# Kernel optimization log

Hardware: AMD Instinct MI355X
Metric: run time of the kernel (lower is better)

## Reference

```python
import jax, jax.numpy as jnp
import numpy as np

B, T, D = 64, 512, 512
K_CODES = 256
K_FUTURE = 2


def _gru(x, w_ih, w_hh, b_ih, b_hh):
    # x: [B,T,D]; PyTorch GRU gate order: r, z, n; weights [3D, D]
    xg = jnp.einsum('btd,gd->btg', x, w_ih) + b_ih  # [B,T,3D] precomputed input gates

    def step(h, xg_t):
        hg = h @ w_hh.T + b_hh                      # [B,3D]
        xr, xz, xn = jnp.split(xg_t, 3, axis=-1)
        hr, hz, hn = jnp.split(hg, 3, axis=-1)
        r = jax.nn.sigmoid(xr + hr)
        z = jax.nn.sigmoid(xz + hz)
        n = jnp.tanh(xn + r * hn)
        h_new = (1.0 - z) * n + z * h
        return h_new, h_new

    h0 = jnp.zeros((x.shape[0], w_hh.shape[1]), x.dtype)
    _, hs = jax.lax.scan(step, h0, jnp.swapaxes(xg, 0, 1))
    return jnp.swapaxes(hs, 0, 1)  # [B,T,D]


def setup_inputs() -> dict:
    key = jax.random.key(0)
    ks = jax.random.split(key, 8)
    return {
        'features': jax.random.normal(ks[0], (B, T, D), jnp.float32),
        'codebook': jax.random.uniform(ks[1], (K_CODES, D), jnp.float32, -0.1, 0.1),
        'w_ih': jax.random.normal(ks[2], (3 * D, D), jnp.float32) * 0.02,
        'w_hh': jax.random.normal(ks[3], (3 * D, D), jnp.float32) * 0.02,
        'b_ih': jax.random.normal(ks[4], (3 * D,), jnp.float32) * 0.02,
        'b_hh': jax.random.normal(ks[5], (3 * D,), jnp.float32) * 0.02,
        'proj_w': jax.random.normal(ks[6], (D, D), jnp.float32) * 0.02,
        'proj_b': jax.random.normal(ks[7], (D,), jnp.float32) * 0.02,
    }


def reference(features, codebook, w_ih, w_hh, b_ih, b_hh, proj_w, proj_b):
    b, t, d = features.shape
    # --- quantize: cdist + argmin + gather (squared dists give same argmin) ---
    flat = features.reshape(-1, d)                              # [B*T, D]
    d2 = (jnp.sum(flat * flat, axis=1, keepdims=True)
          - 2.0 * flat @ codebook.T
          + jnp.sum(codebook * codebook, axis=1))               # [B*T, K]
    indices = jnp.argmin(d2, axis=1)                            # [B*T]
    quantized = codebook[indices].reshape(b, t, d)              # gather
    indices = indices.reshape(b, t)

    # --- context prediction loss ---
    hidden = _gru(quantized, w_ih, w_hh, b_ih, b_hh)            # [B,T,D]
    context_proj = hidden @ proj_w.T + proj_b                   # [B,T,D]
    k_max = min(K_FUTURE, t - 1)
    cp_loss = jnp.float32(0.0)
    for k in range(1, k_max + 1):
        cp_loss = cp_loss + jnp.mean((context_proj[:, :-k] - features[:, k:]) ** 2)
    cp_loss = cp_loss / k_max

    # --- VQ loss (stop_gradient mirrors torch .detach()) ---
    commitment_loss = jnp.mean((jax.lax.stop_gradient(features) - quantized) ** 2)
    codebook_loss = jnp.mean((features - jax.lax.stop_gradient(quantized)) ** 2)
    vq_loss = commitment_loss + 0.25 * codebook_loss

    total_loss = cp_loss + vq_loss
    return quantized, indices, total_loss, cp_loss, vq_loss
```

## Files before the change

kernel.cpp:

```cpp
#include <hip/hip_runtime.h>
#include <hip/hip_bf16.h>

#define B_ 64
#define T_ 512
#define D_ 512
#define K_ 256
#define G3 1536

typedef __attribute__((ext_vector_type(8))) short sh8;
typedef __attribute__((ext_vector_type(4))) short sh4;
typedef __attribute__((ext_vector_type(4))) float fx4;
typedef __attribute__((ext_vector_type(4))) int   ix4;

__device__ __forceinline__ short f2bf(float x) {
  __hip_bfloat16 h = __float2bfloat16(x);
  union { __hip_bfloat16 h; short s; } u; u.h = h; return u.s;
}
__device__ __forceinline__ float sigm(float x) { return 1.f / (1.f + __expf(-x)); }
__device__ __forceinline__ float tanh_fast(float x) {
  float e2 = __expf(-2.f * x);
  return (1.f - e2) / (1.f + e2);
}

__global__ void k_cnorm(const float* __restrict__ cb, double* __restrict__ cn) {
  int c = threadIdx.x;
  if (c < K_) {
    double s = 0.0;
    for (int k = 0; k < D_; ++k) { double v = cb[c * D_ + k]; s += v * v; }
    cn[c] = s;
  }
}

__global__ __launch_bounds__(256) void k_cg(const float* __restrict__ cb,
                                            const float* __restrict__ wih,
                                            const float* __restrict__ bih,
                                            const float* __restrict__ bhh,
                                            float* __restrict__ cg) {
  __shared__ float wl[16][512];
  int j0 = blockIdx.x * 16, c0 = blockIdx.y * 64;
  for (int v = threadIdx.x; v < 16 * 128; v += 256) {
    int r = v >> 7, q = v & 127;
    *(fx4*)&wl[r][q * 4] = *(const fx4*)&wih[(j0 + r) * D_ + q * 4];
  }
  __syncthreads();
  for (int p = threadIdx.x; p < 1024; p += 256) {
    int j = p >> 6, c = c0 + (p & 63);
    fx4 a = {0.f, 0.f, 0.f, 0.f};
    const float* cbr = &cb[c * D_];
    for (int q = 0; q < 128; ++q) {
      fx4 w4 = *(fx4*)&wl[j][q * 4];
      fx4 c4 = *(const fx4*)&cbr[q * 4];
      a += w4 * c4;
    }
    int jg = j0 + j;
    float bias = bih[jg] + (jg < 1024 ? bhh[jg] : 0.f);
    cg[c * G3 + jg] = ((a.x + a.y) + (a.z + a.w)) + bias;
  }
}

__global__ void k_cvt(const float* __restrict__ src, __hip_bfloat16* __restrict__ dst, int n4) {
  int i = blockIdx.x * blockDim.x + threadIdx.x;
  if (i < n4) {
    fx4 v = *(const fx4*)&src[i * 4];
    sh4 o; o[0] = f2bf(v.x); o[1] = f2bf(v.y); o[2] = f2bf(v.z); o[3] = f2bf(v.w);
    *(sh4*)&dst[i * 4] = o;
  }
}

__global__ __launch_bounds__(256) void k_quant(const float* __restrict__ feat,
                                               const float* __restrict__ cb,
                                               const double* __restrict__ cn,
                                               int* __restrict__ idxw,
                                               float* __restrict__ outq,
                                               float* __restrict__ outi,
                                               double* __restrict__ lacc) {
  __shared__ float fl[16][516];
  __shared__ double ss1[16][16], ss2[16][16];
  __shared__ int ii1[16][16], ii2[16][16];
  __shared__ int idxl[16];
  __shared__ float rsv[4];
  int row0 = blockIdx.x * 16;
  int tid = threadIdx.x;
  for (int v = tid; v < 16 * 128; v += 256) {
    int r = v >> 7, q = v & 127;
    *(fx4*)&fl[r][q * 4] = *(const fx4*)&feat[(row0 + r) * D_ + q * 4];
  }
  __syncthreads();
  int r = tid & 15, g = tid >> 4;
  fx4 acc[16];
#pragma unroll
  for (int c = 0; c < 16; ++c) acc[c] = (fx4){0.f, 0.f, 0.f, 0.f};
  for (int ch = 0; ch < 8; ++ch) {
    fx4 fc[16];
#pragma unroll
    for (int q = 0; q < 16; ++q) fc[q] = *(fx4*)&fl[r][ch * 64 + q * 4];
#pragma unroll
    for (int c = 0; c < 16; ++c) {
      const float* cbp = &cb[(g * 16 + c) * D_ + ch * 64];
#pragma unroll
      for (int q = 0; q < 16; ++q) {
        fx4 c4 = *(const fx4*)&cbp[q * 4];
        acc[c] += fc[q] * c4;
      }
    }
  }
  double b1 = 1e300, b2 = 1e300; int i1 = 0, i2 = 0;
#pragma unroll
  for (int c = 0; c < 16; ++c) {
    int ci = g * 16 + c;
    double dot = (double)acc[c].x + acc[c].y + acc[c].z + acc[c].w;
    double s = cn[ci] - 2.0 * dot;
    if (s < b1) { b2 = b1; i2 = i1; b1 = s; i1 = ci; }
    else if (s < b2) { b2 = s; i2 = ci; }
  }
  ss1[r][g] = b1; ss2[r][g] = b2; ii1[r][g] = i1; ii2[r][g] = i2;
  __syncthreads();
  if (tid < 16) {
    int rr = tid;
    double c1 = 1e300, c2 = 1e300; int j1 = 0, j2 = 0;
    for (int g2 = 0; g2 < 16; ++g2) {
      double s = ss1[rr][g2]; int ix = ii1[rr][g2];
      if (s < c1 || (s == c1 && ix < j1)) { c2 = c1; j2 = j1; c1 = s; j1 = ix; }
      else if (s < c2 || (s == c2 && ix < j2)) { c2 = s; j2 = ix; }
      s = ss2[rr][g2]; ix = ii2[rr][g2];
      if (s < c1 || (s == c1 && ix < j1)) { c2 = c1; j2 = j1; c1 = s; j1 = ix; }
      else if (s < c2 || (s == c2 && ix < j2)) { c2 = s; j2 = ix; }
    }
    int pick = j1;
    if (c2 - c1 < 1e-4) {
      double d1 = 0.0, d2 = 0.0;
      for (int k = 0; k < D_; ++k) {
        double fv = fl[rr][k];
        d1 += fv * (double)cb[j1 * D_ + k];
        d2 += fv * (double)cb[j2 * D_ + k];
      }
      double e1 = cn[j1] - 2.0 * d1, e2 = cn[j2] - 2.0 * d2;
      if (e2 < e1 || (e2 == e1 && j2 < j1)) pick = j2;
    }
    idxl[rr] = pick;
    idxw[row0 + rr] = pick;
    outi[row0 + rr] = (float)pick;
  }
  __syncthreads();
  float vs = 0.f;
  for (int v = tid; v < 16 * 128; v += 256) {
    int rr = v >> 7, q = v & 127;
    fx4 c4 = *(const fx4*)&cb[idxl[rr] * D_ + q * 4];
    *(fx4*)&outq[(row0 + rr) * D_ + q * 4] = c4;
    fx4 f4 = *(fx4*)&fl[rr][q * 4];
    fx4 d = f4 - c4;
    vs += d.x * d.x + d.y * d.y + d.z * d.z + d.w * d.w;
  }
#pragma unroll
  for (int off = 32; off > 0; off >>= 1) vs += __shfl_down(vs, off);
  if ((tid & 63) == 0) rsv[tid >> 6] = vs;
  __syncthreads();
  if (tid == 0) atomicAdd(&lacc[2], (double)(rsv[0] + rsv[1] + rsv[2] + rsv[3]));
}

__global__ __launch_bounds__(256, 1) void k_gru(const float* __restrict__ whh,
                                                const float* __restrict__ bhh,
                                                const float* __restrict__ cg,
                                                const int* __restrict__ idx,
                                                __hip_bfloat16* __restrict__ hid,
                                                unsigned int* __restrict__ flag,
                                                int* __restrict__ xcca,
                                                unsigned int* __restrict__ bar0) {
  int bid = blockIdx.x;
  int g = bid & 7, s = bid >> 3;
  int tid = threadIdx.x;
  int w = tid >> 6, lane = tid & 63, l15 = lane & 15, l4 = lane >> 4;

  sh8 A0[16], A1[16], A2[16];
#pragma unroll
  for (int kt = 0; kt < 16; ++kt) {
#pragma unroll
    for (int t3 = 0; t3 < 3; ++t3) {
      const float* wr = &whh[((t3 * 512) + s * 64 + w * 16 + l15) * D_];
      int k0 = kt * 32 + l4 * 8;
      fx4 x = *(const fx4*)&wr[k0];
      fx4 y = *(const fx4*)&wr[k0 + 4];
      sh8 tt;
      tt[0] = f2bf(x.x); tt[1] = f2bf(x.y); tt[2] = f2bf(x.z); tt[3] = f2bf(x.w);
      tt[4] = f2bf(y.x); tt[5] = f2bf(y.y); tt[6] = f2bf(y.z); tt[7] = f2bf(y.w);
      if (t3 == 0) A0[kt] = tt; else if (t3 == 1) A1[kt] = tt; else A2[kt] = tt;
    }
  }

  const bool act = (l15 < 8);
  const int b = l15;
  const int dg0 = s * 64 + w * 16 + l4 * 4;

  fx4 bn = *(const fx4*)&bhh[1024 + dg0];
  fx4 hp = {0.f, 0.f, 0.f, 0.f};

  __shared__ int sh_fast;
  if (tid == 0) {
    int xcc = 0;
    asm volatile("s_getreg_b32 %0, hwreg(HW_REG_XCC_ID)" : "=s"(xcc));
    __hip_atomic_store(&xcca[bid], xcc, __ATOMIC_RELEASE, __HIP_MEMORY_SCOPE_AGENT);
    __hip_atomic_fetch_add(bar0, 1u, __ATOMIC_ACQ_REL, __HIP_MEMORY_SCOPE_AGENT);
    while (__hip_atomic_load(bar0, __ATOMIC_ACQUIRE, __HIP_MEMORY_SCOPE_AGENT) < 64u)
      __builtin_amdgcn_s_sleep(2);
    int x0 = __hip_atomic_load(&xcca[g], __ATOMIC_RELAXED, __HIP_MEMORY_SCOPE_AGENT);
    int f = 1;
    for (int m = 1; m < 8; ++m)
      if (__hip_atomic_load(&xcca[g + 8 * m], __ATOMIC_RELAXED, __HIP_MEMORY_SCOPE_AGENT) != x0)
        f = 0;
    sh_fast = f;
    __threadfence();
  }
  __syncthreads();
  const bool fast = (sh_fast != 0);

  for (int t = 0; t < T_; ++t) {
    fx4 cr = {0, 0, 0, 0}, cz = {0, 0, 0, 0}, cnn = {0, 0, 0, 0};
    if (act) {
      int ci = idx[(g * 8 + b) * T_ + t];
      const float* cgr = &cg[(size_t)ci * G3 + dg0];
      cr  = *(const fx4*)cgr;
      cz  = *(const fx4*)(cgr + 512);
      cnn = *(const fx4*)(cgr + 1024);
    }

    fx4 a0 = {0, 0, 0, 0}, a1 = {0, 0, 0, 0}, a2 = {0, 0, 0, 0};
    if (t > 0) {
      if (tid < 8) {
        const unsigned* fp = &flag[(tid * 8 + g) * 32];
        while (__hip_atomic_load(fp, __ATOMIC_RELAXED, __HIP_MEMORY_SCOPE_AGENT)
               < (unsigned)t) {}
      }
      if (!fast && tid == 0) __threadfence();
      __syncthreads();

      const __hip_bfloat16* hrow =
          &hid[((size_t)(g * 8 + (l15 & 7)) * T_ + (t - 1)) * D_];
#pragma unroll
      for (int kt = 0; kt < 16; ++kt) {
        sh8 bfr = {0, 0, 0, 0, 0, 0, 0, 0};
        if (act) bfr = *(const sh8*)&hrow[kt * 32 + l4 * 8];
        a0 = __builtin_amdgcn_mfma_f32_16x16x32_bf16(A0[kt], bfr, a0, 0, 0, 0);
        a1 = __builtin_amdgcn_mfma_f32_16x16x32_bf16(A1[kt], bfr, a1, 0, 0, 0);
        a2 = __builtin_amdgcn_mfma_f32_16x16x32_bf16(A2[kt], bfr, a2, 0, 0, 0);
      }
    }

    if (act) {
      sh4 hb4;
#pragma unroll
      for (int rg = 0; rg < 4; ++rg) {
        float rr = sigm(cr[rg] + a0[rg]);
        float zz = sigm(cz[rg] + a1[rg]);
        float nn = tanh_fast(cnn[rg] + rr * (a2[rg] + bn[rg]));
        float hv = (1.f - zz) * nn + zz * hp[rg];
        hp[rg] = hv;
        hb4[rg] = f2bf(hv);
      }
      *(sh4*)&hid[((size_t)(g * 8 + b) * T_ + t) * D_ + dg0] = hb4;
    }
    __syncthreads();
    if (tid == 0) {
      if (!fast) __threadfence();
      __hip_atomic_store(&flag[bid * 32], (unsigned)(t + 1), __ATOMIC_RELAXED,
                         __HIP_MEMORY_SCOPE_AGENT);
    }
  }
}

__global__ __launch_bounds__(256) void k_proj(const __hip_bfloat16* __restrict__ hid,
                                              const __hip_bfloat16* __restrict__ pwb,
                                              const float* __restrict__ pb,
                                              const float* __restrict__ feat,
                                              double* __restrict__ lacc) {
  __shared__ char Bl[512 * 64];
  __shared__ char Al[32 * 64];
  __shared__ float rs1[4], rs2[4];
  int Mb = blockIdx.x * 32;
  int tid = threadIdx.x;
  int w = tid >> 6, lane = tid & 63, l15 = lane & 15, l4 = lane >> 4;
  fx4 acc[2][8];
#pragma unroll
  for (int a = 0; a < 2; ++a)
#pragma unroll
    for (int b = 0; b < 8; ++b) acc[a][b] = (fx4){0, 0, 0, 0};

  for (int kc = 0; kc < 16; ++kc) {
    for (int v = tid; v < 2048; v += 256) {
      int rw = v >> 2, sg = v & 3;
      ix4 d = *(const ix4*)&pwb[rw * D_ + kc * 32 + sg * 8];
      *(ix4*)(Bl + rw * 64 + ((sg * 16) ^ ((rw & 7) << 4))) = d;
    }
    if (tid < 128) {
      int rw = tid >> 2, sg = tid & 3;
      ix4 d = *(const ix4*)&hid[(size_t)(Mb + rw) * D_ + kc * 32 + sg * 8];
      *(ix4*)(Al + rw * 64 + ((sg * 16) ^ ((rw & 7) << 4))) = d;
    }
    __syncthreads();
    sh8 af0, af1;
    {
      int m = l15;
      af0 = *(const sh8*)(Al + m * 64 + ((l4 * 16) ^ ((m & 7) << 4)));
      m = 16 + l15;
      af1 = *(const sh8*)(Al + m * 64 + ((l4 * 16) ^ ((m & 7) << 4)));
    }
#pragma unroll
    for (int nt = 0; nt < 8; ++nt) {
      int n = (w * 8 + nt) * 16 + l15;
      sh8 bf = *(const sh8*)(Bl + n * 64 + ((l4 * 16) ^ ((n & 7) << 4)));
      acc[0][nt] = __builtin_amdgcn_mfma_f32_16x16x32_bf16(af0, bf, acc[0][nt], 0, 0, 0);
      acc[1][nt] = __builtin_amdgcn_mfma_f32_16x16x32_bf16(af1, bf, acc[1][nt], 0, 0, 0);
    }
    __syncthreads();
  }

  float s1 = 0.f, s2 = 0.f;
#pragma unroll
  for (int mt = 0; mt < 2; ++mt) {
#pragma unroll
    for (int nt = 0; nt < 8; ++nt) {
      int n = (w * 8 + nt) * 16 + l15;
      float bias = pb[n];
#pragma unroll
      for (int rg = 0; rg < 4; ++rg) {
        int m = Mb + mt * 16 + l4 * 4 + rg;
        float val = acc[mt][nt][rg] + bias;
        int t = m & (T_ - 1);
        if (t < T_ - 1) { float d = val - feat[(size_t)(m + 1) * D_ + n]; s1 += d * d; }
        if (t < T_ - 2) { float d = val - feat[(size_t)(m + 2) * D_ + n]; s2 += d * d; }
      }
    }
  }
#pragma unroll
  for (int off = 32; off > 0; off >>= 1) {
    s1 += __shfl_down(s1, off);
    s2 += __shfl_down(s2, off);
  }
  if (lane == 0) { rs1[w] = s1; rs2[w] = s2; }
  __syncthreads();
  if (tid == 0) {
    atomicAdd(&lacc[0], (double)rs1[0] + rs1[1] + rs1[2] + rs1[3]);
    atomicAdd(&lacc[1], (double)rs2[0] + rs2[1] + rs2[2] + rs2[3]);
  }
}

__global__ void k_fin(const double* __restrict__ lacc, float* __restrict__ outl) {
  if (threadIdx.x == 0) {
    double cp = 0.5 * (lacc[0] / ((double)B_ * (T_ - 1) * D_) +
                       lacc[1] / ((double)B_ * (T_ - 2) * D_));
    double vq = 1.25 * lacc[2] / ((double)B_ * T_ * D_);
    outl[0] = (float)(cp + vq);
    outl[1] = (float)cp;
    outl[2] = (float)vq;
  }
}

extern "C" void kernel_launch(void* const* d_in, const int* in_sizes, int n_in,
                              void* d_out, int out_size, void* d_ws, size_t ws_size,
                              hipStream_t stream) {
  (void)in_sizes; (void)n_in; (void)out_size; (void)ws_size;
  const float* feat = (const float*)d_in[0];
  const float* cb   = (const float*)d_in[1];
  const float* wih  = (const float*)d_in[2];
  const float* whh  = (const float*)d_in[3];
  const float* bih  = (const float*)d_in[4];
  const float* bhh  = (const float*)d_in[5];
  const float* pw   = (const float*)d_in[6];
  const float* pb   = (const float*)d_in[7];

  float* out  = (float*)d_out;
  float* outq = out;
  float* outi = out + (size_t)B_ * T_ * D_;
  float* outl = outi + B_ * T_;

  char* ws = (char*)d_ws;
  size_t o = 0;
  auto alloc = [&](size_t sz) { void* p = ws + o; o += (sz + 255) & ~(size_t)255; return p; };
  float*          cg   = (float*)alloc(sizeof(float) * K_ * G3);
  double*         cn   = (double*)alloc(sizeof(double) * K_);
  int*            idxw = (int*)alloc(sizeof(int) * B_ * T_);
  __hip_bfloat16* pwb  = (__hip_bfloat16*)alloc(sizeof(__hip_bfloat16) * D_ * D_);
  double*         lacc = (double*)alloc(sizeof(double) * 4);
  unsigned*       flag = (unsigned*)alloc(sizeof(unsigned) * 64 * 32);
  int*            xcca = (int*)alloc(sizeof(int) * 64);
  unsigned*       bar0 = (unsigned*)alloc(sizeof(unsigned) * 4);
  __hip_bfloat16* hid  = (__hip_bfloat16*)alloc(sizeof(__hip_bfloat16) * (size_t)B_ * T_ * D_);

  hipMemsetAsync(lacc, 0, sizeof(double) * 4, stream);
  hipMemsetAsync(flag, 0, sizeof(unsigned) * 64 * 32, stream);
  hipMemsetAsync(xcca, 0, sizeof(int) * 64, stream);
  hipMemsetAsync(bar0, 0, sizeof(unsigned) * 4, stream);

  hipLaunchKernelGGL(k_cnorm, dim3(1), dim3(256), 0, stream, cb, cn);
  hipLaunchKernelGGL(k_cg, dim3(96, 4), dim3(256), 0, stream, cb, wih, bih, bhh, cg);
  hipLaunchKernelGGL(k_cvt, dim3(256), dim3(256), 0, stream, pw, pwb, D_ * D_ / 4);
  hipLaunchKernelGGL(k_quant, dim3(2048), dim3(256), 0, stream, feat, cb, cn, idxw, outq, outi, lacc);
  hipLaunchKernelGGL(k_gru, dim3(64), dim3(256), 0, stream, whh, bhh, cg, idxw, hid, flag, xcca, bar0);
  hipLaunchKernelGGL(k_proj, dim3(1024), dim3(256), 0, stream, hid, pwb, pb, feat, lacc);
  hipLaunchKernelGGL(k_fin, dim3(1), dim3(64), 0, stream, lacc, outl);
}
```

Measured before the change: 3.223 ms.

## Launch surplus GRU blocks and assign roles by XCC for same-die groups

The GRU kernel now launches 256 blocks and dynamically assigns the 64 working roles so that each group of 8 cooperating blocks lands on the same XCC where possible, with surplus blocks exiting. This lets groups use the fast path that skips the global fence. Per-step flag polling over 8 peers is replaced with a single per-group atomic counter barrier. It also prefetches the next code index and raises wave priority. The cost is extra launched blocks, an initial global rendezvous, and a fall-back path for groups that span XCCs.

```diff
diff --git a/kernel.cpp b/kernel.cpp
--- a/kernel.cpp
+++ b/kernel.cpp
@@ -163,12 +163,54 @@
                                                 const float* __restrict__ cg,
                                                 const int* __restrict__ idx,
                                                 __hip_bfloat16* __restrict__ hid,
-                                                unsigned int* __restrict__ flag,
-                                                int* __restrict__ xcca,
-                                                unsigned int* __restrict__ bar0) {
-  int bid = blockIdx.x;
-  int g = bid & 7, s = bid >> 3;
+                                                unsigned int* __restrict__ bar,
+                                                unsigned int* __restrict__ coord) {
   int tid = threadIdx.x;
+  __shared__ int sh_role, sh_fast;
+
+  if (tid == 0) {
+    int xcc = 0;
+    asm volatile("s_getreg_b32 %0, hwreg(HW_REG_XCC_ID)" : "=s"(xcc));
+    xcc &= 7;
+    unsigned slot = __hip_atomic_fetch_add(&coord[xcc], 1u, __ATOMIC_RELAXED,
+                                           __HIP_MEMORY_SCOPE_AGENT);
+    __hip_atomic_fetch_add(&coord[16], 1u, __ATOMIC_ACQ_REL, __HIP_MEMORY_SCOPE_AGENT);
+    while (__hip_atomic_load(&coord[16], __ATOMIC_ACQUIRE, __HIP_MEMORY_SCOPE_AGENT)
+           < (unsigned)gridDim.x)
+      __builtin_amdgcn_s_sleep(2);
+
+    int role = -1;
+    if (slot < 8u) {
+      role = xcc * 8 + (int)slot;
+    } else {
+      for (int x = 0; x < 8 && role < 0; ++x) {
+        unsigned cx = __hip_atomic_load(&coord[x], __ATOMIC_RELAXED,
+                                        __HIP_MEMORY_SCOPE_AGENT);
+        unsigned have = cx < 8u ? cx : 8u;
+        if (have < 8u) {
+          unsigned s2 = __hip_atomic_fetch_add(&coord[8 + x], 1u, __ATOMIC_RELAXED,
+                                               __HIP_MEMORY_SCOPE_AGENT);
+          if (s2 < 8u - have) role = x * 8 + (int)(have + s2);
+        }
+      }
+    }
+    sh_role = role;
+    int fst = 0;
+    if (role >= 0) {
+      unsigned cgx = __hip_atomic_load(&coord[role >> 3], __ATOMIC_RELAXED,
+                                       __HIP_MEMORY_SCOPE_AGENT);
+      fst = (cgx >= 8u) ? 1 : 0;
+    }
+    sh_fast = fst;
+    __threadfence();
+  }
+  __syncthreads();
+  const int role = sh_role;
+  if (role < 0) return;
+  const bool fast = (sh_fast != 0);
+  const int g = role >> 3, s = role & 7;
+
+  __builtin_amdgcn_s_setprio(1);
   int w = tid >> 6, lane = tid & 63, l15 = lane & 15, l4 = lane >> 4;
 
   sh8 A0[16], A1[16], A2[16];
@@ -188,53 +230,31 @@
   }
 
   const bool act = (l15 < 8);
-  const int b = l15;
+  const int b = l15 & 7;
   const int dg0 = s * 64 + w * 16 + l4 * 4;
 
   fx4 bn = *(const fx4*)&bhh[1024 + dg0];
   fx4 hp = {0.f, 0.f, 0.f, 0.f};
 
-  __shared__ int sh_fast;
-  if (tid == 0) {
-    int xcc = 0;
-    asm volatile("s_getreg_b32 %0, hwreg(HW_REG_XCC_ID)" : "=s"(xcc));
-    __hip_atomic_store(&xcca[bid], xcc, __ATOMIC_RELEASE, __HIP_MEMORY_SCOPE_AGENT);
-    __hip_atomic_fetch_add(bar0, 1u, __ATOMIC_ACQ_REL, __HIP_MEMORY_SCOPE_AGENT);
-    while (__hip_atomic_load(bar0, __ATOMIC_ACQUIRE, __HIP_MEMORY_SCOPE_AGENT) < 64u)
-      __builtin_amdgcn_s_sleep(2);
-    int x0 = __hip_atomic_load(&xcca[g], __ATOMIC_RELAXED, __HIP_MEMORY_SCOPE_AGENT);
-    int f = 1;
-    for (int m = 1; m < 8; ++m)
-      if (__hip_atomic_load(&xcca[g + 8 * m], __ATOMIC_RELAXED, __HIP_MEMORY_SCOPE_AGENT) != x0)
-        f = 0;
-    sh_fast = f;
-    __threadfence();
-  }
-  __syncthreads();
-  const bool fast = (sh_fast != 0);
+  unsigned* const barg = &bar[g * 32];
+
+  int ci = act ? idx[(g * 8 + b) * T_] : 0;
 
   for (int t = 0; t < T_; ++t) {
     fx4 cr = {0, 0, 0, 0}, cz = {0, 0, 0, 0}, cnn = {0, 0, 0, 0};
+    int ci_nx = 0;
     if (act) {
-      int ci = idx[(g * 8 + b) * T_ + t];
       const float* cgr = &cg[(size_t)ci * G3 + dg0];
       cr  = *(const fx4*)cgr;
       cz  = *(const fx4*)(cgr + 512);
       cnn = *(const fx4*)(cgr + 1024);
+      if (t + 1 < T_) ci_nx = idx[(g * 8 + b) * T_ + t + 1];
     }
 
     fx4 a0 = {0, 0, 0, 0}, a1 = {0, 0, 0, 0}, a2 = {0, 0, 0, 0};
     if (t > 0) {
-      if (tid < 8) {
-        const unsigned* fp = &flag[(tid * 8 + g) * 32];
-        while (__hip_atomic_load(fp, __ATOMIC_RELAXED, __HIP_MEMORY_SCOPE_AGENT)
-               < (unsigned)t) {}
-      }
-      if (!fast && tid == 0) __threadfence();
-      __syncthreads();
-
       const __hip_bfloat16* hrow =
-          &hid[((size_t)(g * 8 + (l15 & 7)) * T_ + (t - 1)) * D_];
+          &hid[((size_t)(g * 8 + b) * T_ + (t - 1)) * D_];
 #pragma unroll
       for (int kt = 0; kt < 16; ++kt) {
         sh8 bfr = {0, 0, 0, 0, 0, 0, 0, 0};
@@ -258,12 +278,18 @@
       }
       *(sh4*)&hid[((size_t)(g * 8 + b) * T_ + t) * D_ + dg0] = hb4;
     }
+    ci = ci_nx;
+
     __syncthreads();
     if (tid == 0) {
       if (!fast) __threadfence();
-      __hip_atomic_store(&flag[bid * 32], (unsigned)(t + 1), __ATOMIC_RELAXED,
-                         __HIP_MEMORY_SCOPE_AGENT);
-    }
+      __hip_atomic_fetch_add(barg, 1u, __ATOMIC_RELAXED, __HIP_MEMORY_SCOPE_AGENT);
+      unsigned tgt = 8u * (unsigned)(t + 1);
+      while (__hip_atomic_load(barg, __ATOMIC_RELAXED, __HIP_MEMORY_SCOPE_AGENT) < tgt)
+        __builtin_amdgcn_s_sleep(1);
+      if (!fast) __threadfence();
+    }
+    __syncthreads();
   }
 }
 
@@ -375,26 +401,24 @@
   char* ws = (char*)d_ws;
   size_t o = 0;
   auto alloc = [&](size_t sz) { void* p = ws + o; o += (sz + 255) & ~(size_t)255; return p; };
-  float*          cg   = (float*)alloc(sizeof(float) * K_ * G3);
-  double*         cn   = (double*)alloc(sizeof(double) * K_);
-  int*            idxw = (int*)alloc(sizeof(int) * B_ * T_);
-  __hip_bfloat16* pwb  = (__hip_bfloat16*)alloc(sizeof(__hip_bfloat16) * D_ * D_);
-  double*         lacc = (double*)alloc(sizeof(double) * 4);
-  unsigned*       flag = (unsigned*)alloc(sizeof(unsigned) * 64 * 32);
-  int*            xcca = (int*)alloc(sizeof(int) * 64);
-  unsigned*       bar0 = (unsigned*)alloc(sizeof(unsigned) * 4);
-  __hip_bfloat16* hid  = (__hip_bfloat16*)alloc(sizeof(__hip_bfloat16) * (size_t)B_ * T_ * D_);
-
-  hipMemsetAsync(lacc, 0, sizeof(double) * 4, stream);
-  hipMemsetAsync(flag, 0, sizeof(unsigned) * 64 * 32, stream);
-  hipMemsetAsync(xcca, 0, sizeof(int) * 64, stream);
-  hipMemsetAsync(bar0, 0, sizeof(unsigned) * 4, stream);
+  float*          cg    = (float*)alloc(sizeof(float) * K_ * G3);
+  double*         cn    = (double*)alloc(sizeof(double) * K_);
+  int*            idxw  = (int*)alloc(sizeof(int) * B_ * T_);
+  __hip_bfloat16* pwb   = (__hip_bfloat16*)alloc(sizeof(__hip_bfloat16) * D_ * D_);
+  double*         lacc  = (double*)alloc(sizeof(double) * 4);
+  unsigned*       bar   = (unsigned*)alloc(sizeof(unsigned) * 8 * 32);
+  unsigned*       coord = (unsigned*)alloc(sizeof(unsigned) * 32);
+  __hip_bfloat16* hid   = (__hip_bfloat16*)alloc(sizeof(__hip_bfloat16) * (size_t)B_ * T_ * D_);
+
+  hipMemsetAsync(lacc,  0, sizeof(double) * 4, stream);
+  hipMemsetAsync(bar,   0, sizeof(unsigned) * 8 * 32, stream);
+  hipMemsetAsync(coord, 0, sizeof(unsigned) * 32, stream);
 
   hipLaunchKernelGGL(k_cnorm, dim3(1), dim3(256), 0, stream, cb, cn);
   hipLaunchKernelGGL(k_cg, dim3(96, 4), dim3(256), 0, stream, cb, wih, bih, bhh, cg);
   hipLaunchKernelGGL(k_cvt, dim3(256), dim3(256), 0, stream, pw, pwb, D_ * D_ / 4);
   hipLaunchKernelGGL(k_quant, dim3(2048), dim3(256), 0, stream, feat, cb, cn, idxw, outq, outi, lacc);
-  hipLaunchKernelGGL(k_gru, dim3(64), dim3(256), 0, stream, whh, bhh, cg, idxw, hid, flag, xcca, bar0);
+  hipLaunchKernelGGL(k_gru, dim3(256), dim3(256), 0, stream, whh, bhh, cg, idxw, hid, bar, coord);
   hipLaunchKernelGGL(k_proj, dim3(1024), dim3(256), 0, stream, hid, pwb, pb, feat, lacc);
   hipLaunchKernelGGL(k_fin, dim3(1), dim3(64), 0, stream, lacc, outl);
 }
```

Result: slower. 3.290 ms (+2.1%).
